# Kernel tuning notes

Hardware: AMD Instinct MI355X
Metric: run time of the kernel (lower is better)

Reference implementation:

```python
import jax, jax.numpy as jnp
import numpy as np

DIM = 512
HEADS = 8
DIM_HEAD = 64
DIM_INNER = HEADS * DIM_HEAD
SCALE = DIM_HEAD ** -0.5


def setup_inputs() -> dict:
    key = jax.random.key(0)
    ks = jax.random.split(key, 8)
    b, n = 2, 1024
    x = jax.random.normal(ks[0], (b, n, DIM), dtype=jnp.float32)
    w = lambda k, i, o: jax.random.normal(k, (i, o), dtype=jnp.float32) * 0.02
    return {
        'x': x,
        'w_q_u': w(ks[1], DIM, DIM_INNER),
        'w_k_u': w(ks[2], DIM, DIM_INNER),
        'w_v_u': w(ks[3], DIM, DIM_INNER),
        'w_q_c': w(ks[4], DIM, DIM_INNER),
        'w_k_c': w(ks[5], DIM, DIM_INNER),
        'w_v_c': w(ks[6], DIM, DIM_INNER),
        'w_out': w(ks[7], DIM_INNER, DIM),
    }


def reference(x, w_q_u, w_k_u, w_v_u, w_q_c, w_k_c, w_v_c, w_out):
    b, n, _ = x.shape

    def proj(w):  # [b,n,dim] -> [b,h,n,d]
        return (x @ w).reshape(b, n, HEADS, DIM_HEAD).transpose(0, 2, 1, 3)

    q_u, k_u, v_u = proj(w_q_u), proj(w_k_u), proj(w_v_u)
    q_c, k_c, v_c = proj(w_q_c), proj(w_k_c), proj(w_v_c)

    idx = jnp.arange(n)
    causal = idx[:, None] >= idx[None, :]  # tril ones (binary causal mask)

    # term1 = (q_c @ v_u^T) * scale, zeroed above diagonal
    term1 = jnp.einsum('bhid,bhjd->bhij', q_c, v_u) * SCALE
    term1 = term1 * causal.astype(term1.dtype)

    # sigmoid term: (q_u @ k_u^T)*scale with lookahead mask tril(-inf, diag=0)
    logits_u = jnp.einsum('bhid,bhjd->bhij', q_u, k_u) * SCALE
    sig = jax.nn.sigmoid(jnp.where(causal, -jnp.inf, logits_u))

    # S_u[i,k] = sum_j term1[i,j] * sig[k,j]
    S_u = jnp.einsum('bhij,bhkj->bhik', term1, sig)

    # S_c: causal-masked QK
    S_c = jnp.einsum('bhid,bhjd->bhij', q_c, k_c) * SCALE
    S_c = jnp.where(causal, S_c, -jnp.inf)

    final_scores = S_c - jax.nn.silu(S_u)
    attn = jax.nn.softmax(final_scores, axis=-1)
    out = jnp.einsum('bhij,bhjd->bhid', attn, v_c)  # [b,h,n,d]
    out = out.transpose(0, 2, 1, 3).reshape(b, n, DIM_INNER)
    return out @ w_out
```

## Files before the change

### kernel.cpp

```cpp
#include <hip/hip_runtime.h>
#include <math.h>


typedef __bf16 bf16x8 __attribute__((ext_vector_type(8)));
typedef float f32x4 __attribute__((ext_vector_type(4)));

#define SCALE 0.125f

#define GLL(g, l) __builtin_amdgcn_global_load_lds(                         \
    (const __attribute__((address_space(1))) void*)(g),                     \
    (__attribute__((address_space(3))) void*)(l), 16, 0, 0)

__device__ __forceinline__ unsigned short f2bf(float f){
  unsigned int x = __builtin_bit_cast(unsigned int, f);
  unsigned int r = (x + 0x7fffu + ((x >> 16) & 1u)) >> 16;
  return (unsigned short)r;
}
__device__ __forceinline__ f32x4 mfma16(bf16x8 a, bf16x8 b, f32x4 c){
  return __builtin_amdgcn_mfma_f32_16x16x32_bf16(a, b, c, 0, 0, 0);
}
__device__ __forceinline__ bf16x8 ld8(const unsigned short* p){
  return *(const bf16x8*)p;
}

__global__ __launch_bounds__(256) void k_prep_x(
    const float* __restrict__ x, unsigned short* __restrict__ xb){
  int i = blockIdx.x * 256 + threadIdx.x;
  float4 v = ((const float4*)x)[i];
  ushort4 o; o.x = f2bf(v.x); o.y = f2bf(v.y); o.z = f2bf(v.z); o.w = f2bf(v.w);
  ((ushort4*)xb)[i] = o;
}

__global__ __launch_bounds__(256) void k_prep_w(
    const float* __restrict__ w0, const float* __restrict__ w1,
    const float* __restrict__ w2, const float* __restrict__ w3,
    const float* __restrict__ w4, const float* __restrict__ w5,
    const float* __restrict__ w6, unsigned short* __restrict__ wT){
  __shared__ float lds[64 * 65];
  int bx = blockIdx.x;
  int mat = bx >> 6, tile = bx & 63, tr = tile >> 3, tc = tile & 7;
  int k0 = tr * 64, c0 = tc * 64;
  const float* src;
  switch (mat){
    case 0: src = w0; break; case 1: src = w1; break; case 2: src = w2; break;
    case 3: src = w3; break; case 4: src = w4; break; case 5: src = w5; break;
    default: src = w6; break;
  }
  int t = threadIdx.x;
#pragma unroll
  for (int i = 0; i < 4; ++i){
    int r = (t >> 4) + i * 16, c4 = (t & 15) * 4;
    float4 v = *(const float4*)(src + (size_t)(k0 + r) * 512 + c0 + c4);
    lds[r * 65 + c4 + 0] = v.x; lds[r * 65 + c4 + 1] = v.y;
    lds[r * 65 + c4 + 2] = v.z; lds[r * 65 + c4 + 3] = v.w;
  }
  __syncthreads();
  unsigned short* dst = wT + (size_t)mat * 262144;
#pragma unroll
  for (int i = 0; i < 4; ++i){
    int oc = (t >> 4) + i * 16;
    int kq = (t & 15) * 4;
    ushort4 o;
    o.x = f2bf(lds[(kq + 0) * 65 + oc]);
    o.y = f2bf(lds[(kq + 1) * 65 + oc]);
    o.z = f2bf(lds[(kq + 2) * 65 + oc]);
    o.w = f2bf(lds[(kq + 3) * 65 + oc]);
    *(ushort4*)(dst + (size_t)(c0 + oc) * 512 + k0 + kq) = o;
  }
}

__global__ __launch_bounds__(256) void k_proj(
    const unsigned short* __restrict__ xb, const unsigned short* __restrict__ wT,
    unsigned short* __restrict__ P){
  __shared__ unsigned short sA[128 * 32], sB[128 * 32];
  int t = threadIdx.x, lane = t & 63, l16 = lane & 15, quad = lane >> 4;
  int w = t >> 6, wm = w >> 1, wn = w & 1;
  int bx = blockIdx.x;
  int mt = bx / 24, nt = bx - mt * 24;
  int M0 = mt * 128, N0 = nt * 128;
  int matb = N0 >> 9;
  int nin = N0 & 511;
  int srow = (lane >> 2), scol = (lane & 3) * 8;
  const unsigned short* gA = xb + (size_t)(M0 + w*32 + srow) * 512 + scol;
  const unsigned short* gB = wT + (size_t)matb * 262144
                               + (size_t)(nin + w*32 + srow) * 512 + scol;
  unsigned short* lA = sA + (w*32) * 32;
  unsigned short* lB = sB + (w*32) * 32;
  f32x4 acc[4][4] = {};
  for (int k0 = 0; k0 < 512; k0 += 32){
    GLL(gA + k0,            lA);
    GLL(gA + k0 + 16*512,   lA + 16*32);
    GLL(gB + k0,            lB);
    GLL(gB + k0 + 16*512,   lB + 16*32);
    __syncthreads();
    bf16x8 aw[4], ax[4];
#pragma unroll
    for (int fi = 0; fi < 4; ++fi)
      aw[fi] = *(const bf16x8*)(sB + (wn*64 + fi*16 + l16) * 32 + quad * 8);
#pragma unroll
    for (int mi = 0; mi < 4; ++mi)
      ax[mi] = *(const bf16x8*)(sA + (wm*64 + mi*16 + l16) * 32 + quad * 8);
#pragma unroll
    for (int fi = 0; fi < 4; ++fi)
#pragma unroll
      for (int mi = 0; mi < 4; ++mi)
        acc[fi][mi] = mfma16(aw[fi], ax[mi], acc[fi][mi]);
    __syncthreads();
  }
#pragma unroll
  for (int fi = 0; fi < 4; ++fi)
#pragma unroll
    for (int mi = 0; mi < 4; ++mi){
      int row = M0 + wm*64 + mi*16 + l16;
      int b_ = row >> 10, n_ = row & 1023;
      int c0 = N0 + wn*64 + fi*16 + quad*4;
      int h = (c0 & 511) >> 6, d = c0 & 63;
      int bh = b_*8 + h;
      ushort4 o;
      o.x = f2bf(acc[fi][mi][0]); o.y = f2bf(acc[fi][mi][1]);
      o.z = f2bf(acc[fi][mi][2]); o.w = f2bf(acc[fi][mi][3]);
      *(ushort4*)(P + (size_t)(matb*16 + bh) * 65536 + (size_t)n_ * 64 + d) = o;
    }
}

__global__ __launch_bounds__(256) void k_vct(
    const unsigned short* __restrict__ P5, unsigned short* __restrict__ vcT){
  __shared__ unsigned short lds[64 * 72];
  int bh = blockIdx.x >> 4, nt = blockIdx.x & 15;
  int N0 = nt * 64;
  const unsigned short* src = P5 + (size_t)bh * 65536 + (size_t)N0 * 64;
  int t = threadIdx.x;
#pragma unroll
  for (int it = 0; it < 2; ++it){
    int id = it * 256 + t;
    int r = id >> 3, c8 = (id & 7) * 8;
    ushort4 v0 = *(const ushort4*)(src + r * 64 + c8);
    ushort4 v1 = *(const ushort4*)(src + r * 64 + c8 + 4);
    *(ushort4*)(lds + r * 72 + c8) = v0;
    *(ushort4*)(lds + r * 72 + c8 + 4) = v1;
  }
  __syncthreads();
  unsigned short* dst = vcT + (size_t)bh * 65536;
#pragma unroll
  for (int it = 0; it < 2; ++it){
    int id = it * 256 + t;
    int dd = id >> 3, n8 = (id & 7) * 8;
    ushort4 a, b;
    a.x = lds[(n8+0)*72 + dd]; a.y = lds[(n8+1)*72 + dd];
    a.z = lds[(n8+2)*72 + dd]; a.w = lds[(n8+3)*72 + dd];
    b.x = lds[(n8+4)*72 + dd]; b.y = lds[(n8+5)*72 + dd];
    b.z = lds[(n8+6)*72 + dd]; b.w = lds[(n8+7)*72 + dd];
    *(ushort4*)(dst + (size_t)dd * 1024 + N0 + n8) = a;
    *(ushort4*)(dst + (size_t)dd * 1024 + N0 + n8 + 4) = b;
  }
}

__global__ __launch_bounds__(256) void k_qk(
    const unsigned short* __restrict__ P,
    unsigned short* __restrict__ term1, unsigned short* __restrict__ sig){
  int gw = (blockIdx.x * 256 + threadIdx.x) >> 6;
  int lane = threadIdx.x & 63, l16 = lane & 15, quad = lane >> 4;
  int bhm = gw / 576;
  int idx = gw - bhm * 576;
  int bh = bhm >> 1, mat = bhm & 1;
  int B = 0;
  while (idx >= 8 * (B + 1) * (B + 2)) ++B;
  int r2 = idx - 8 * B * (B + 1);
  int per = 2 * (B + 1);
  int mt_in = r2 / per, sub = r2 - mt_in * per;
  int m0 = (B * 8 + mt_in) * 16, n0 = sub * 64;
  if (mat){ m0 = 1008 - m0; n0 = 960 - n0; }
  unsigned short* out = (mat ? sig : term1) + (size_t)bh * 1048576;
  int row = m0 + l16;
  bool zero_tile = mat ? (n0 + 63 <= m0) : (n0 > m0 + 15);
  if (zero_tile){
    ushort4 z = {0, 0, 0, 0};
#pragma unroll
    for (int f = 0; f < 4; ++f)
      *(ushort4*)(out + (size_t)row * 1024 + n0 + f*16 + quad*4) = z;
    return;
  }
  const unsigned short* A  = P + (size_t)((mat ? 0 : 3)*16 + bh) * 65536;
  const unsigned short* Bt = P + (size_t)((mat ? 1 : 2)*16 + bh) * 65536;
  f32x4 acc[4] = {};
  for (int k0 = 0; k0 < 64; k0 += 32){
    bf16x8 bi = ld8(A + (size_t)(m0 + l16) * 64 + k0 + quad * 8);
#pragma unroll
    for (int f = 0; f < 4; ++f){
      bf16x8 aj = ld8(Bt + (size_t)(n0 + f*16 + l16) * 64 + k0 + quad * 8);
      acc[f] = mfma16(aj, bi, acc[f]);
    }
  }
#pragma unroll
  for (int f = 0; f < 4; ++f){
    int c0 = n0 + f*16 + quad*4;
    ushort4 o;
#pragma unroll
    for (int r = 0; r < 4; ++r){
      int col = c0 + r;
      float v = acc[f][r] * SCALE;
      unsigned short res;
      if (mat == 0) res = (col <= row) ? f2bf(v) : (unsigned short)0;
      else          res = (col >  row) ? f2bf(1.f / (1.f + expf(-v))) : (unsigned short)0;
      ((unsigned short*)&o)[r] = res;
    }
    *(ushort4*)(out + (size_t)row * 1024 + c0) = o;
  }
}

__global__ __launch_bounds__(256) void k_scores(
    const unsigned short* __restrict__ P, const unsigned short* __restrict__ term1,
    const unsigned short* __restrict__ sig, float* __restrict__ fin){
  __shared__ unsigned short sA[128 * 32], sB[128 * 32];
  int t = threadIdx.x;
  int bh = blockIdx.x & 15, tt = blockIdx.x >> 4;
  int k = 1, T = 0;
  while (tt >= T + k){ T += k; ++k; }
  int delta = 8 - k;
  int tj = tt - T, ti = tj + delta;
  int M0 = ti * 128, N0 = tj * 128;
  size_t sbase = (size_t)bh * 1048576;
  int lane = t & 63, l16 = lane & 15, quad = lane >> 4;
  int w = t >> 6, wm = w >> 1, wn = w & 1;
  int srow = (lane >> 2), scol = (lane & 3) * 8;
  unsigned short* lA = sA + (w*32) * 32;
  unsigned short* lB = sB + (w*32) * 32;
  f32x4 acc_u[4][4] = {};
  f32x4 acc_c[4][4] = {};
  {
    const unsigned short* gA = term1 + sbase + (size_t)(M0 + w*32 + srow) * 1024 + scol;
    const unsigned short* gB = sig   + sbase + (size_t)(N0 + w*32 + srow) * 1024 + scol;
    int steps = (delta + 1) * 4;
    for (int s = 0; s < steps; ++s){
      int j0 = N0 + s * 32;
      GLL(gA + j0,             lA);
      GLL(gA + j0 + 16*1024,   lA + 16*32);
      GLL(gB + j0,             lB);
      GLL(gB + j0 + 16*1024,   lB + 16*32);
      __syncthreads();
      bf16x8 af[4], bfr[4];
#pragma unroll
      for (int mi = 0; mi < 4; ++mi)
        af[mi] = *(const bf16x8*)(sA + (wm*64 + mi*16 + l16) * 32 + quad * 8);
#pragma unroll
      for (int fi = 0; fi < 4; ++fi)
        bfr[fi] = *(const bf16x8*)(sB + (wn*64 + fi*16 + l16) * 32 + quad * 8);
#pragma unroll
      for (int fi = 0; fi < 4; ++fi)
#pragma unroll
        for (int mi = 0; mi < 4; ++mi)
          acc_u[fi][mi] = mfma16(bfr[fi], af[mi], acc_u[fi][mi]);
      __syncthreads();
    }
  }
  {
    const unsigned short* Qc = P + (size_t)(3*16 + bh) * 65536;
    const unsigned short* Kc = P + (size_t)(4*16 + bh) * 65536;
    const unsigned short* gA = Qc + (size_t)(M0 + w*32 + srow) * 64 + scol;
    const unsigned short* gB = Kc + (size_t)(N0 + w*32 + srow) * 64 + scol;
    for (int s = 0; s < 2; ++s){
      int k0 = s * 32;
      GLL(gA + k0,           lA);
      GLL(gA + k0 + 16*64,   lA + 16*32);
      GLL(gB + k0,           lB);
      GLL(gB + k0 + 16*64,   lB + 16*32);
      __syncthreads();
      bf16x8 af[4], bfr[4];
#pragma unroll
      for (int mi = 0; mi < 4; ++mi)
        af[mi] = *(const bf16x8*)(sA + (wm*64 + mi*16 + l16) * 32 + quad * 8);
#pragma unroll
      for (int fi = 0; fi < 4; ++fi)
        bfr[fi] = *(const bf16x8*)(sB + (wn*64 + fi*16 + l16) * 32 + quad * 8);
#pragma unroll
      for (int fi = 0; fi < 4; ++fi)
#pragma unroll
        for (int mi = 0; mi < 4; ++mi)
          acc_c[fi][mi] = mfma16(bfr[fi], af[mi], acc_c[fi][mi]);
      __syncthreads();
    }
  }
  float* out = fin + sbase;
#pragma unroll
  for (int fi = 0; fi < 4; ++fi)
#pragma unroll
    for (int mi = 0; mi < 4; ++mi){
      int row = M0 + wm*64 + mi*16 + l16;
      int c0 = N0 + wn*64 + fi*16 + quad*4;
      float4 o;
#pragma unroll
      for (int r = 0; r < 4; ++r){
        int col = c0 + r;
        float su = acc_u[fi][mi][r];
        float v = acc_c[fi][mi][r] * SCALE - su / (1.f + expf(-su));
        ((float*)&o)[r] = (col > row) ? -INFINITY : v;
      }
      *(float4*)(out + (size_t)row * 1024 + c0) = o;
    }
}

__global__ __launch_bounds__(256) void k_softmax(
    const float* __restrict__ fin, unsigned short* __restrict__ probs){
  int w = threadIdx.x >> 6, lane = threadIdx.x & 63;
  int row = blockIdx.x * 4 + w;
  int rloc = row & 1023;
  const float* p = fin + (size_t)row * 1024;
  float4 v[4];
  float m = -INFINITY;
#pragma unroll
  for (int i = 0; i < 4; ++i){
    float4 x = ((const float4*)p)[i * 64 + lane];
    int c0 = (i * 64 + lane) * 4;
    v[i].x = (c0 + 0 <= rloc) ? x.x : -INFINITY;
    v[i].y = (c0 + 1 <= rloc) ? x.y : -INFINITY;
    v[i].z = (c0 + 2 <= rloc) ? x.z : -INFINITY;
    v[i].w = (c0 + 3 <= rloc) ? x.w : -INFINITY;
    m = fmaxf(m, fmaxf(fmaxf(v[i].x, v[i].y), fmaxf(v[i].z, v[i].w)));
  }
#pragma unroll
  for (int off = 32; off > 0; off >>= 1) m = fmaxf(m, __shfl_xor(m, off));
  float s = 0.f;
#pragma unroll
  for (int i = 0; i < 4; ++i){
    v[i].x = expf(v[i].x - m); v[i].y = expf(v[i].y - m);
    v[i].z = expf(v[i].z - m); v[i].w = expf(v[i].w - m);
    s += v[i].x + v[i].y + v[i].z + v[i].w;
  }
#pragma unroll
  for (int off = 32; off > 0; off >>= 1) s += __shfl_xor(s, off);
  float inv = 1.f / s;
  unsigned short* q = probs + (size_t)row * 1024;
#pragma unroll
  for (int i = 0; i < 4; ++i){
    ushort4 o;
    o.x = f2bf(v[i].x * inv); o.y = f2bf(v[i].y * inv);
    o.z = f2bf(v[i].z * inv); o.w = f2bf(v[i].w * inv);
    ((ushort4*)q)[i * 64 + lane] = o;
  }
}

__global__ __launch_bounds__(256) void k_pv(
    const unsigned short* __restrict__ probs, const unsigned short* __restrict__ vcT,
    unsigned short* __restrict__ O){
  __shared__ float red[4][1024];
  int t = threadIdx.x, lane = t & 63, l16 = lane & 15, quad = lane >> 4, w = t >> 6;
  int bh = blockIdx.x & 15, mt = 63 - (blockIdx.x >> 4);
  int m0 = mt * 16;
  const unsigned short* A  = probs + (size_t)bh * 1048576;
  const unsigned short* Bt = vcT + (size_t)bh * 65536;
  int ktot = (m0 + 16 + 31) >> 5;
  int per = (ktot + 3) >> 2;
  int s0 = w * per, s1 = min(s0 + per, ktot);
  f32x4 acc[4] = {};
  for (int s = s0; s < s1; ++s){
    int k0 = s * 32;
    bf16x8 a = ld8(A + (size_t)(m0 + l16) * 1024 + k0 + quad * 8);
#pragma unroll
    for (int fi = 0; fi < 4; ++fi){
      bf16x8 b = ld8(Bt + (size_t)(fi*16 + l16) * 1024 + k0 + quad * 8);
      acc[fi] = mfma16(a, b, acc[fi]);
    }
  }
#pragma unroll
  for (int fi = 0; fi < 4; ++fi)
#pragma unroll
    for (int r = 0; r < 4; ++r)
      red[w][(quad*4 + r) * 64 + fi*16 + l16] = acc[fi][r];
  __syncthreads();
  float4 a0 = ((const float4*)red[0])[t];
  float4 a1 = ((const float4*)red[1])[t];
  float4 a2 = ((const float4*)red[2])[t];
  float4 a3 = ((const float4*)red[3])[t];
  ushort4 o;
  o.x = f2bf(a0.x + a1.x + a2.x + a3.x);
  o.y = f2bf(a0.y + a1.y + a2.y + a3.y);
  o.z = f2bf(a0.z + a1.z + a2.z + a3.z);
  o.w = f2bf(a0.w + a1.w + a2.w + a3.w);
  int e = t * 4, row = e >> 6, col = e & 63;
  *(ushort4*)(O + (size_t)bh * 65536 + (size_t)(m0 + row) * 64 + col) = o;
}

__global__ __launch_bounds__(256) void k_out(
    const unsigned short* __restrict__ O, const unsigned short* __restrict__ woT,
    float* __restrict__ out){
  __shared__ float red[4][1024];
  int t = threadIdx.x, lane = t & 63, l16 = lane & 15, quad = lane >> 4, w = t >> 6;
  int mt = blockIdx.x >> 3, nt = blockIdx.x & 7;
  int m0 = mt * 16, n0 = nt * 64;
  int r_ = m0 + l16, b_ = r_ >> 10, n_ = r_ & 1023;
  f32x4 acc[4] = {};
#pragma unroll
  for (int s = 0; s < 4; ++s){
    int kk = w * 128 + s * 32 + quad * 8;
    int h = kk >> 6, dd = kk & 63;
    bf16x8 a = ld8(O + (size_t)(b_*8 + h) * 65536 + (size_t)n_ * 64 + dd);
#pragma unroll
    for (int fi = 0; fi < 4; ++fi){
      bf16x8 b = ld8(woT + (size_t)(n0 + fi*16 + l16) * 512 + kk);
      acc[fi] = mfma16(a, b, acc[fi]);
    }
  }
#pragma unroll
  for (int fi = 0; fi < 4; ++fi)
#pragma unroll
    for (int r = 0; r < 4; ++r)
      red[w][(quad*4 + r) * 64 + fi*16 + l16] = acc[fi][r];
  __syncthreads();
  float4 a0 = ((const float4*)red[0])[t];
  float4 a1 = ((const float4*)red[1])[t];
  float4 a2 = ((const float4*)red[2])[t];
  float4 a3 = ((const float4*)red[3])[t];
  float4 o;
  o.x = a0.x + a1.x + a2.x + a3.x;
  o.y = a0.y + a1.y + a2.y + a3.y;
  o.z = a0.z + a1.z + a2.z + a3.z;
  o.w = a0.w + a1.w + a2.w + a3.w;
  int e = t * 4, row = e >> 6, col = e & 63;
  *(float4*)(out + (size_t)(m0 + row) * 512 + n0 + col) = o;
}

extern "C" void kernel_launch(void* const* d_in, const int* in_sizes, int n_in,
                              void* d_out, int out_size, void* d_ws, size_t ws_size,
                              hipStream_t stream){
  const float* x = (const float*)d_in[0];
  float* out = (float*)d_out;
  unsigned short* ws = (unsigned short*)d_ws;

  unsigned short* wT    = ws;
  unsigned short* xb    = wT    + (size_t)7  * 262144;
  unsigned short* P     = xb    + (size_t)1048576;
  unsigned short* vcT   = P     + (size_t)96 * 65536;
  unsigned short* term1 = vcT   + (size_t)16 * 65536;
  unsigned short* sig   = term1 + (size_t)16 * 1048576;
  unsigned short* O     = sig   + (size_t)16 * 1048576;
  float*          fin   = (float*)(O + (size_t)16 * 65536);
  unsigned short* probs = term1;

  k_prep_x<<<1024, 256, 0, stream>>>(x, xb);
  k_prep_w<<<448, 256, 0, stream>>>(
      (const float*)d_in[1], (const float*)d_in[2], (const float*)d_in[3],
      (const float*)d_in[4], (const float*)d_in[5], (const float*)d_in[6],
      (const float*)d_in[7], wT);
  k_proj<<<384, 256, 0, stream>>>(xb, wT, P);
  k_vct<<<256, 256, 0, stream>>>(P + (size_t)5*16*65536, vcT);
  k_qk<<<4608, 256, 0, stream>>>(P, term1, sig);
  k_scores<<<576, 256, 0, stream>>>(P, term1, sig, fin);
  k_softmax<<<4096, 256, 0, stream>>>(fin, probs);
  k_pv<<<1024, 256, 0, stream>>>(probs, vcT, O);
  k_out<<<1024, 256, 0, stream>>>(O, wT + (size_t)6 * 262144, out);
}
```

Before: 193.0 us.

## Fuse softmax into PV kernel via LDS and merge prep kernels

Softmax is now computed inside the PV kernel: each block normalizes its 16 rows of fp32 scores, reading only the causal prefix, and writes bf16 probabilities to LDS for the MFMA loop. This removes the separate softmax launch and the global round trip of the probability matrix. The x and weight prep kernels are also merged into one launch to cut launch overhead. In exchange, each block holds 16 float4 registers per thread and about 33KB of LDS, which may lower occupancy.

```diff
diff --git a/kernel.cpp b/kernel.cpp
--- a/kernel.cpp
+++ b/kernel.cpp
@@ -23,21 +23,23 @@
   return *(const bf16x8*)p;
 }
 
-__global__ __launch_bounds__(256) void k_prep_x(
-    const float* __restrict__ x, unsigned short* __restrict__ xb){
-  int i = blockIdx.x * 256 + threadIdx.x;
-  float4 v = ((const float4*)x)[i];
-  ushort4 o; o.x = f2bf(v.x); o.y = f2bf(v.y); o.z = f2bf(v.z); o.w = f2bf(v.w);
-  ((ushort4*)xb)[i] = o;
-}
-
-__global__ __launch_bounds__(256) void k_prep_w(
+__global__ __launch_bounds__(256) void k_prep(
+    const float* __restrict__ x,
     const float* __restrict__ w0, const float* __restrict__ w1,
     const float* __restrict__ w2, const float* __restrict__ w3,
     const float* __restrict__ w4, const float* __restrict__ w5,
-    const float* __restrict__ w6, unsigned short* __restrict__ wT){
+    const float* __restrict__ w6,
+    unsigned short* __restrict__ xb, unsigned short* __restrict__ wT){
+  int t = threadIdx.x;
+  if (blockIdx.x < 1024){
+    int i = blockIdx.x * 256 + t;
+    float4 v = ((const float4*)x)[i];
+    ushort4 o; o.x = f2bf(v.x); o.y = f2bf(v.y); o.z = f2bf(v.z); o.w = f2bf(v.w);
+    ((ushort4*)xb)[i] = o;
+    return;
+  }
   __shared__ float lds[64 * 65];
-  int bx = blockIdx.x;
+  int bx = blockIdx.x - 1024;
   int mat = bx >> 6, tile = bx & 63, tr = tile >> 3, tc = tile & 7;
   int k0 = tr * 64, c0 = tc * 64;
   const float* src;
@@ -46,7 +48,6 @@
     case 3: src = w3; break; case 4: src = w4; break; case 5: src = w5; break;
     default: src = w6; break;
   }
-  int t = threadIdx.x;
 #pragma unroll
   for (int i = 0; i < 4; ++i){
     int r = (t >> 4) + i * 16, c4 = (t & 15) * 4;
@@ -299,78 +300,87 @@
     }
 }
 
-__global__ __launch_bounds__(256) void k_softmax(
-    const float* __restrict__ fin, unsigned short* __restrict__ probs){
-  int w = threadIdx.x >> 6, lane = threadIdx.x & 63;
-  int row = blockIdx.x * 4 + w;
-  int rloc = row & 1023;
-  const float* p = fin + (size_t)row * 1024;
-  float4 v[4];
-  float m = -INFINITY;
-#pragma unroll
-  for (int i = 0; i < 4; ++i){
-    float4 x = ((const float4*)p)[i * 64 + lane];
-    int c0 = (i * 64 + lane) * 4;
-    v[i].x = (c0 + 0 <= rloc) ? x.x : -INFINITY;
-    v[i].y = (c0 + 1 <= rloc) ? x.y : -INFINITY;
-    v[i].z = (c0 + 2 <= rloc) ? x.z : -INFINITY;
-    v[i].w = (c0 + 3 <= rloc) ? x.w : -INFINITY;
-    m = fmaxf(m, fmaxf(fmaxf(v[i].x, v[i].y), fmaxf(v[i].z, v[i].w)));
-  }
-#pragma unroll
-  for (int off = 32; off > 0; off >>= 1) m = fmaxf(m, __shfl_xor(m, off));
-  float s = 0.f;
-#pragma unroll
-  for (int i = 0; i < 4; ++i){
-    v[i].x = expf(v[i].x - m); v[i].y = expf(v[i].y - m);
-    v[i].z = expf(v[i].z - m); v[i].w = expf(v[i].w - m);
-    s += v[i].x + v[i].y + v[i].z + v[i].w;
-  }
-#pragma unroll
-  for (int off = 32; off > 0; off >>= 1) s += __shfl_xor(s, off);
-  float inv = 1.f / s;
-  unsigned short* q = probs + (size_t)row * 1024;
-#pragma unroll
-  for (int i = 0; i < 4; ++i){
-    ushort4 o;
-    o.x = f2bf(v[i].x * inv); o.y = f2bf(v[i].y * inv);
-    o.z = f2bf(v[i].z * inv); o.w = f2bf(v[i].w * inv);
-    ((ushort4*)q)[i * 64 + lane] = o;
-  }
-}
-
-__global__ __launch_bounds__(256) void k_pv(
-    const unsigned short* __restrict__ probs, const unsigned short* __restrict__ vcT,
+__global__ __launch_bounds__(256) void k_pv_soft(
+    const float* __restrict__ fin, const unsigned short* __restrict__ vcT,
     unsigned short* __restrict__ O){
-  __shared__ float red[4][1024];
-  int t = threadIdx.x, lane = t & 63, l16 = lane & 15, quad = lane >> 4, w = t >> 6;
+  __shared__ __align__(16) unsigned char smem[16 * 1032 * 2];
+  unsigned short* lp = (unsigned short*)smem;
+  float* red = (float*)smem;
+  int t = threadIdx.x;
   int bh = blockIdx.x & 15, mt = 63 - (blockIdx.x >> 4);
   int m0 = mt * 16;
-  const unsigned short* A  = probs + (size_t)bh * 1048576;
+  int kceil = ((m0 + 16 + 31) >> 5) << 5;
+  {
+    int rl = t >> 4, sub = t & 15;
+    int rloc = m0 + rl;
+    const float* p = fin + (size_t)bh * 1048576 + (size_t)rloc * 1024;
+    float4 v[16];
+    float m = -INFINITY;
+#pragma unroll
+    for (int i = 0; i < 16; ++i){
+      int c4 = (sub + 16*i) * 4;
+      if (c4 < kceil){
+        float4 xv = *(const float4*)(p + c4);
+        v[i].x = (c4 + 0 <= rloc) ? xv.x : -INFINITY;
+        v[i].y = (c4 + 1 <= rloc) ? xv.y : -INFINITY;
+        v[i].z = (c4 + 2 <= rloc) ? xv.z : -INFINITY;
+        v[i].w = (c4 + 3 <= rloc) ? xv.w : -INFINITY;
+        m = fmaxf(m, fmaxf(fmaxf(v[i].x, v[i].y), fmaxf(v[i].z, v[i].w)));
+      }
+    }
+#pragma unroll
+    for (int off = 1; off < 16; off <<= 1) m = fmaxf(m, __shfl_xor(m, off));
+    float s = 0.f;
+#pragma unroll
+    for (int i = 0; i < 16; ++i){
+      int c4 = (sub + 16*i) * 4;
+      if (c4 < kceil){
+        v[i].x = expf(v[i].x - m); v[i].y = expf(v[i].y - m);
+        v[i].z = expf(v[i].z - m); v[i].w = expf(v[i].w - m);
+        s += v[i].x + v[i].y + v[i].z + v[i].w;
+      }
+    }
+#pragma unroll
+    for (int off = 1; off < 16; off <<= 1) s += __shfl_xor(s, off);
+    float inv = 1.f / s;
+#pragma unroll
+    for (int i = 0; i < 16; ++i){
+      int c4 = (sub + 16*i) * 4;
+      if (c4 < kceil){
+        ushort4 o;
+        o.x = f2bf(v[i].x * inv); o.y = f2bf(v[i].y * inv);
+        o.z = f2bf(v[i].z * inv); o.w = f2bf(v[i].w * inv);
+        *(ushort4*)(lp + rl * 1032 + c4) = o;
+      }
+    }
+  }
+  __syncthreads();
+  int lane = t & 63, l16 = lane & 15, quad = lane >> 4, w = t >> 6;
   const unsigned short* Bt = vcT + (size_t)bh * 65536;
-  int ktot = (m0 + 16 + 31) >> 5;
+  int ktot = kceil >> 5;
   int per = (ktot + 3) >> 2;
   int s0 = w * per, s1 = min(s0 + per, ktot);
   f32x4 acc[4] = {};
   for (int s = s0; s < s1; ++s){
     int k0 = s * 32;
-    bf16x8 a = ld8(A + (size_t)(m0 + l16) * 1024 + k0 + quad * 8);
+    bf16x8 a = *(const bf16x8*)(lp + l16 * 1032 + k0 + quad * 8);
 #pragma unroll
     for (int fi = 0; fi < 4; ++fi){
       bf16x8 b = ld8(Bt + (size_t)(fi*16 + l16) * 1024 + k0 + quad * 8);
       acc[fi] = mfma16(a, b, acc[fi]);
     }
   }
+  __syncthreads();
 #pragma unroll
   for (int fi = 0; fi < 4; ++fi)
 #pragma unroll
     for (int r = 0; r < 4; ++r)
-      red[w][(quad*4 + r) * 64 + fi*16 + l16] = acc[fi][r];
-  __syncthreads();
-  float4 a0 = ((const float4*)red[0])[t];
-  float4 a1 = ((const float4*)red[1])[t];
-  float4 a2 = ((const float4*)red[2])[t];
-  float4 a3 = ((const float4*)red[3])[t];
+      red[w * 1024 + (quad*4 + r) * 64 + fi*16 + l16] = acc[fi][r];
+  __syncthreads();
+  float4 a0 = ((const float4*)(red + 0*1024))[t];
+  float4 a1 = ((const float4*)(red + 1*1024))[t];
+  float4 a2 = ((const float4*)(red + 2*1024))[t];
+  float4 a3 = ((const float4*)(red + 3*1024))[t];
   ushort4 o;
   o.x = f2bf(a0.x + a1.x + a2.x + a3.x);
   o.y = f2bf(a0.y + a1.y + a2.y + a3.y);
@@ -434,18 +444,16 @@
   unsigned short* sig   = term1 + (size_t)16 * 1048576;
   unsigned short* O     = sig   + (size_t)16 * 1048576;
   float*          fin   = (float*)(O + (size_t)16 * 65536);
-  unsigned short* probs = term1;
-
-  k_prep_x<<<1024, 256, 0, stream>>>(x, xb);
-  k_prep_w<<<448, 256, 0, stream>>>(
+
+  k_prep<<<1472, 256, 0, stream>>>(
+      x,
       (const float*)d_in[1], (const float*)d_in[2], (const float*)d_in[3],
       (const float*)d_in[4], (const float*)d_in[5], (const float*)d_in[6],
-      (const float*)d_in[7], wT);
+      (const float*)d_in[7], xb, wT);
   k_proj<<<384, 256, 0, stream>>>(xb, wT, P);
   k_vct<<<256, 256, 0, stream>>>(P + (size_t)5*16*65536, vcT);
   k_qk<<<4608, 256, 0, stream>>>(P, term1, sig);
   k_scores<<<576, 256, 0, stream>>>(P, term1, sig, fin);
-  k_softmax<<<4096, 256, 0, stream>>>(fin, probs);
-  k_pv<<<1024, 256, 0, stream>>>(probs, vcT, O);
+  k_pv_soft<<<1024, 256, 0, stream>>>(fin, vcT, O);
   k_out<<<1024, 256, 0, stream>>>(O, wT + (size_t)6 * 262144, out);
 }
```

Result: faster. 180.6 us (-6.4%).
